# Optimization experiments

Hardware: AMD Instinct MI355X
Metric: run time of the kernel (lower is better)

The kernel has to match this reference:

```python
import jax, jax.numpy as jnp
import numpy as np
import itertools

B, K, H, W = 64, 5, 320, 320
EPS = 1e-6
# All K! permutations (exact equivalent of scipy.linear_sum_assignment for KxK cost)
PERMS = np.array(list(itertools.permutations(range(K))), dtype=np.int32)  # [P, K]


def setup_inputs() -> dict:
    key = jax.random.key(0)
    k1, k2, k3 = jax.random.split(key, 3)
    return {
        "fg_logits": jax.random.normal(k1, (B, 1, H, W), dtype=jnp.float32),
        "slot_logits": jax.random.normal(k2, (B, K, H, W), dtype=jnp.float32),
        "target": jax.random.uniform(k3, (B, 1, H, W), dtype=jnp.float32),
    }


def reference(fg_logits, slot_logits, target):
    fg = target[:, 0]            # [B,H,W]
    bg = 1.0 - fg                # [B,H,W]
    # targets_b: index 0 = FG mask, 1..K-1 = BG mask (duplicated)  -> [B,K,H,W]
    targets = jnp.concatenate([fg[:, None], jnp.broadcast_to(bg[:, None], (B, K - 1, H, W))], axis=1)

    # IoU cost matrix on detached sigmoid probs (matches .detach())
    probs = jax.lax.stop_gradient(jax.nn.sigmoid(slot_logits))
    s = probs.reshape(B, K, -1)        # [B,K,N]
    t = targets.reshape(B, K, -1)      # [B,K,N]
    inter = jnp.einsum('bkn,bjn->bkj', s, t)           # [B,K,K]
    union = s.sum(-1)[:, :, None] + t.sum(-1)[:, None, :] - inter + EPS
    cost = 1.0 - inter / union                          # [B,K,K]

    # Exact Hungarian via brute force over K! permutations (K small)
    perms = jnp.asarray(PERMS)                          # [P,K]
    rows = jnp.arange(K)[None, :]                       # [1,K]
    perm_cost = cost[:, rows, perms].sum(-1)            # [B,P]
    best_perm = perms[jnp.argmin(perm_cost, axis=1)]    # [B,K] col_ind per sample

    # aligned[i] = targets[col_ind[i]]; targets[j] is fg iff j == 0
    is_fg = (best_perm == 0)[:, :, None, None]          # [B,K,1,1]
    aligned = jnp.where(is_fg, fg[:, None], bg[:, None])  # [B,K,H,W]

    # Stable sigmoid-BCE with logits, mean-reduced per sample then averaged over B
    x = slot_logits
    bce = jnp.maximum(x, 0.0) - x * aligned + jnp.log1p(jnp.exp(-jnp.abs(x)))
    return bce.mean()
```

## Files before the change

kernel.cpp:

```cpp
#include <hip/hip_runtime.h>


#define BB 64
#define KK 5
#define NPIX 102400
#define CHUNKS 20
#define CHUNK_PIX 5120
#define ITERS 20
#define THREADS 320
#define REC 32

__global__ void hung_pass1(const float* __restrict__ slot,
                           const float* __restrict__ tgt,
                           float* __restrict__ ws)
{
    const int b    = blockIdx.y;
    const int cx   = blockIdx.x;
    const int w    = threadIdx.x >> 6;
    const int lane = threadIdx.x & 63;

    const float* t  = tgt  + (size_t)b * NPIX + cx * CHUNK_PIX;
    const float* xk = slot + ((size_t)b * KK + w) * NPIX + cx * CHUNK_PIX;

    float X = 0.f, XF = 0.f, S = 0.f, SF = 0.f, PX = 0.f, Tf = 0.f;

    #pragma unroll 4
    for (int i = 0; i < ITERS; ++i) {
        const int off = i * 256 + lane * 4;
        const float4 fg4 = *reinterpret_cast<const float4*>(t + off);
        const float4 x4  = *reinterpret_cast<const float4*>(xk + off);
        const float fgv[4] = {fg4.x, fg4.y, fg4.z, fg4.w};
        const float xv[4]  = {x4.x, x4.y, x4.z, x4.w};
        #pragma unroll
        for (int j = 0; j < 4; ++j) {
            const float x  = xv[j];
            const float fg = fgv[j];
            const float e  = __expf(-fabsf(x));
            const float L  = __logf(1.0f + e);
            const float d  = L + fmaxf(-x, 0.0f);
            const float s  = __expf(-d);
            PX += d;
            X  += x;
            XF  = fmaf(x, fg, XF);
            S  += s;
            SF  = fmaf(s, fg, SF);
            Tf += fg;
        }
    }

    float v[6] = {X, XF, S, SF, PX, Tf};
    #pragma unroll
    for (int j = 0; j < 6; ++j) {
        float x = v[j];
        #pragma unroll
        for (int off = 32; off > 0; off >>= 1) x += __shfl_down(x, off, 64);
        v[j] = x;
    }
    if (lane == 0) {
        float* rec = ws + (size_t)(cx * BB + b) * REC;
        rec[w]      = v[0];
        rec[5 + w]  = v[1];
        rec[10 + w] = v[2];
        rec[15 + w] = v[3];
        rec[20 + w] = v[4];
        if (w == 0) rec[25] = v[5];
    }
}

__global__ __launch_bounds__(256) void hung_pass2(const float* __restrict__ ws,
                                                  float* __restrict__ out)
{
    __shared__ float red[BB][26];
    for (int idx = threadIdx.x; idx < BB * 26; idx += 256) {
        const int b = idx / 26, j = idx - b * 26;
        float s = 0.f;
        #pragma unroll 4
        for (int c = 0; c < CHUNKS; ++c)
            s += ws[(size_t)(c * BB + b) * REC + j];
        red[b][j] = s;
    }
    __syncthreads();
    if (threadIdx.x < 64) {
        const int b = threadIdx.x;
        const float* v = red[b];
        const float Tf = v[25];
        const float Tb = (float)NPIX - Tf;
        float best = 3.402823466e+38f; int kb = 0;
        float xfsum = 0.f, px = 0.f;
        #pragma unroll
        for (int k = 0; k < KK; ++k) {
            const float Sv = v[10 + k], Iv = v[15 + k];
            const float cf = 1.f - Iv / (Sv + Tf - Iv + 1e-6f);
            const float Ib = Sv - Iv;
            const float cb = 1.f - Ib / (Sv + Tb - Ib + 1e-6f);
            const float dd = cf - cb;
            if (dd < best) { best = dd; kb = k; }
            xfsum += v[5 + k];
            px    += v[20 + k];
        }
        float res = px + xfsum - (2.f * v[5 + kb] - v[kb]);
        #pragma unroll
        for (int off = 32; off > 0; off >>= 1) res += __shfl_down(res, off, 64);
        if (b == 0) out[0] = res * (1.0f / 32768000.0f);
    }
}

extern "C" void kernel_launch(void* const* d_in, const int* in_sizes, int n_in,
                              void* d_out, int out_size, void* d_ws, size_t ws_size,
                              hipStream_t stream) {
    const float* slot = (const float*)d_in[1];
    const float* tgt  = (const float*)d_in[2];
    float* out = (float*)d_out;
    float* ws  = (float*)d_ws;

    dim3 grid(CHUNKS, BB);
    hung_pass1<<<grid, THREADS, 0, stream>>>(slot, tgt, ws);
    hung_pass2<<<1, 256, 0, stream>>>(ws, out);
}
```

Measured before the change: 234.2 us.

## Repartition pass1 grid into per-(batch,slot) quarter blocks with block reduction

```diff
diff --git a/kernel.cpp b/kernel.cpp
--- a/kernel.cpp
+++ b/kernel.cpp
@@ -4,30 +4,32 @@
 #define BB 64
 #define KK 5
 #define NPIX 102400
-#define CHUNKS 20
-#define CHUNK_PIX 5120
-#define ITERS 20
-#define THREADS 320
-#define REC 32
+#define QUARTERS 4
+#define SEG 25600
+#define ITERS 25
+#define THREADS 256
+#define REC 8
+#define NBLK (BB * KK * QUARTERS)
 
 __global__ void hung_pass1(const float* __restrict__ slot,
                            const float* __restrict__ tgt,
                            float* __restrict__ ws)
 {
-    const int b    = blockIdx.y;
-    const int cx   = blockIdx.x;
-    const int w    = threadIdx.x >> 6;
-    const int lane = threadIdx.x & 63;
+    const int bid = blockIdx.x;
+    const int q   = bid & (QUARTERS - 1);
+    const int bk  = bid >> 2;
+    const int b   = bk / KK;
 
-    const float* t  = tgt  + (size_t)b * NPIX + cx * CHUNK_PIX;
-    const float* xk = slot + ((size_t)b * KK + w) * NPIX + cx * CHUNK_PIX;
+    const float* xk = slot + (size_t)bk * NPIX + q * SEG;
+    const float* t  = tgt  + (size_t)b  * NPIX + q * SEG;
 
     float X = 0.f, XF = 0.f, S = 0.f, SF = 0.f, PX = 0.f, Tf = 0.f;
 
-    #pragma unroll 4
+    const int base = threadIdx.x * 4;
+    #pragma unroll 5
     for (int i = 0; i < ITERS; ++i) {
-        const int off = i * 256 + lane * 4;
-        const float4 fg4 = *reinterpret_cast<const float4*>(t + off);
+        const int off = base + i * (THREADS * 4);
+        const float4 fg4 = *reinterpret_cast<const float4*>(t  + off);
         const float4 x4  = *reinterpret_cast<const float4*>(xk + off);
         const float fgv[4] = {fg4.x, fg4.y, fg4.z, fg4.w};
         const float xv[4]  = {x4.x, x4.y, x4.z, x4.w};
@@ -56,49 +58,57 @@
         for (int off = 32; off > 0; off >>= 1) x += __shfl_down(x, off, 64);
         v[j] = x;
     }
+    __shared__ float red[THREADS / 64][6];
+    const int lane = threadIdx.x & 63;
+    const int w    = threadIdx.x >> 6;
     if (lane == 0) {
-        float* rec = ws + (size_t)(cx * BB + b) * REC;
-        rec[w]      = v[0];
-        rec[5 + w]  = v[1];
-        rec[10 + w] = v[2];
-        rec[15 + w] = v[3];
-        rec[20 + w] = v[4];
-        if (w == 0) rec[25] = v[5];
+        #pragma unroll
+        for (int j = 0; j < 6; ++j) red[w][j] = v[j];
+    }
+    __syncthreads();
+    if (threadIdx.x < 6) {
+        const int j = threadIdx.x;
+        ws[(size_t)bid * REC + j] =
+            red[0][j] + red[1][j] + red[2][j] + red[3][j];
     }
 }
 
-__global__ __launch_bounds__(256) void hung_pass2(const float* __restrict__ ws,
+__global__ __launch_bounds__(320) void hung_pass2(const float* __restrict__ ws,
                                                   float* __restrict__ out)
 {
-    __shared__ float red[BB][26];
-    for (int idx = threadIdx.x; idx < BB * 26; idx += 256) {
-        const int b = idx / 26, j = idx - b * 26;
-        float s = 0.f;
-        #pragma unroll 4
-        for (int c = 0; c < CHUNKS; ++c)
-            s += ws[(size_t)(c * BB + b) * REC + j];
-        red[b][j] = s;
+    __shared__ float red[BB][KK][6];
+    const int t = threadIdx.x;
+    if (t < BB * KK) {
+        float v[6] = {0, 0, 0, 0, 0, 0};
+        #pragma unroll
+        for (int q = 0; q < QUARTERS; ++q) {
+            const float* p = ws + (size_t)(t * QUARTERS + q) * REC;
+            #pragma unroll
+            for (int j = 0; j < 6; ++j) v[j] += p[j];
+        }
+        const int b = t / KK, k = t - b * KK;
+        #pragma unroll
+        for (int j = 0; j < 6; ++j) red[b][k][j] = v[j];
     }
     __syncthreads();
-    if (threadIdx.x < 64) {
-        const int b = threadIdx.x;
-        const float* v = red[b];
-        const float Tf = v[25];
+    if (t < BB) {
+        const int b = t;
+        const float Tf = red[b][0][5];
         const float Tb = (float)NPIX - Tf;
         float best = 3.402823466e+38f; int kb = 0;
         float xfsum = 0.f, px = 0.f;
         #pragma unroll
         for (int k = 0; k < KK; ++k) {
-            const float Sv = v[10 + k], Iv = v[15 + k];
+            const float Sv = red[b][k][2], Iv = red[b][k][3];
             const float cf = 1.f - Iv / (Sv + Tf - Iv + 1e-6f);
             const float Ib = Sv - Iv;
             const float cb = 1.f - Ib / (Sv + Tb - Ib + 1e-6f);
             const float dd = cf - cb;
             if (dd < best) { best = dd; kb = k; }
-            xfsum += v[5 + k];
-            px    += v[20 + k];
+            xfsum += red[b][k][1];
+            px    += red[b][k][4];
         }
-        float res = px + xfsum - (2.f * v[5 + kb] - v[kb]);
+        float res = px + xfsum - (2.f * red[b][kb][1] - red[b][kb][0]);
         #pragma unroll
         for (int off = 32; off > 0; off >>= 1) res += __shfl_down(res, off, 64);
         if (b == 0) out[0] = res * (1.0f / 32768000.0f);
@@ -113,7 +123,6 @@
     float* out = (float*)d_out;
     float* ws  = (float*)d_ws;
 
-    dim3 grid(CHUNKS, BB);
-    hung_pass1<<<grid, THREADS, 0, stream>>>(slot, tgt, ws);
-    hung_pass2<<<1, 256, 0, stream>>>(ws, out);
+    hung_pass1<<<NBLK, THREADS, 0, stream>>>(slot, tgt, ws);
+    hung_pass2<<<1, 320, 0, stream>>>(ws, out);
 }
```

After: 222.7 us. 4.9% less time.
